# Kernel tuning notes

Hardware: AMD Instinct MI355X
Metric: run time of the kernel (lower is better)

The kernel has to match this reference:

```python
import jax, jax.numpy as jnp
import numpy as np

B, T, K, H = 8, 1024, 128, 8
TOP_K = 64
KS = 5  # conv kernel size for Q/K
DN = ('NCH', 'OIH', 'NCH')


def setup_inputs() -> dict:
    key = jax.random.key(0)
    ks = jax.random.split(key, 9)
    s = 0.05
    return {
        'x': jax.random.normal(ks[0], (B, T, K), jnp.float32),
        'Wq': jax.random.normal(ks[1], (K * H, K, KS), jnp.float32) * s,
        'bq': jax.random.normal(ks[2], (K * H,), jnp.float32) * s,
        'Wk': jax.random.normal(ks[3], (K * H, K, KS), jnp.float32) * s,
        'bk': jax.random.normal(ks[4], (K * H,), jnp.float32) * s,
        'Wv': jax.random.normal(ks[5], (K * H, K, 1), jnp.float32) * s,
        'bv': jax.random.normal(ks[6], (K * H,), jnp.float32) * s,
        'Wu': jax.random.normal(ks[7], (K, K * H), jnp.float32) * s,
        'bu': jax.random.normal(ks[8], (K,), jnp.float32) * s,
    }


def _prep(z, b, k, h, t, scale):
    # z: (b, k*h, t) conv output; torch view(b,k,h,t) then transposes -> (b,h,t,k)
    z = z.reshape(b, k, h, t)
    z = jnp.transpose(z, (0, 2, 3, 1)) * scale  # (b, h, t, k)
    # torch: transpose(1,2).contiguous().view(b*h, t, k) -- replicate exactly
    z = jnp.transpose(z, (0, 2, 1, 3)).reshape(b * h, t, k)
    return z


def reference(x, Wq, bq, Wk, bk, Wv, bv, Wu, bu):
    b, t, k = x.shape
    h = H
    xc = jnp.transpose(x, (0, 2, 1))  # (b, k, t)
    # causal left-pad KS-1 for Q/K convs; V is pointwise (kernel 1)
    q = jax.lax.conv_general_dilated(xc, Wq, (1,), [(KS - 1, 0)], dimension_numbers=DN) + bq[None, :, None]
    kk = jax.lax.conv_general_dilated(xc, Wk, (1,), [(KS - 1, 0)], dimension_numbers=DN) + bk[None, :, None]
    v = jax.lax.conv_general_dilated(xc, Wv, (1,), [(0, 0)], dimension_numbers=DN) + bv[None, :, None]
    scale = k ** -0.25
    q = _prep(q, b, k, h, t, scale)
    kk = _prep(kk, b, k, h, t, scale)
    v = _prep(v, b, k, h, t, 1.0)
    w = jnp.einsum('btk,bsk->bts', q, kk)  # (b*h, t, t)
    # top-k sparsification: keep entries >= k-th largest per row, else row min
    largest, _ = jax.lax.top_k(w, TOP_K)
    thresh = jnp.min(largest, axis=-1, keepdims=True)
    row_min = jnp.min(w, axis=-1, keepdims=True)
    w = jnp.where(w >= thresh, w, row_min)
    # causal mask (strict upper triangle -> -inf)
    causal = jnp.triu(jnp.ones((t, t), bool), 1)
    w = jnp.where(causal[None], -jnp.inf, w)
    w = jax.nn.softmax(w, axis=-1)
    out = jnp.einsum('bts,bsk->btk', w, v)  # (b*h, t, k)
    out = out.reshape(b, h, t, k)
    out = jnp.transpose(out, (0, 2, 1, 3)).reshape(b, t, k * h)
    return out @ Wu.T + bu
```

## Files before the change

### kernel.cpp

```cpp
#include <hip/hip_runtime.h>
#include <hip/hip_fp16.h>
#include <cstdint>

using f16 = _Float16;
typedef __attribute__((ext_vector_type(8))) _Float16 f16x8;
typedef __attribute__((ext_vector_type(4))) _Float16 f16x4;
typedef __attribute__((ext_vector_type(4))) float f32x4;

#define MFMA16(a, b, c) __builtin_amdgcn_mfma_f32_16x16x32_f16((a), (b), (c), 0, 0, 0)

__device__ __forceinline__ f16x8 ldfrag(const f16* p) { return *(const f16x8*)p; }

__device__ __forceinline__ void dma16(const f16* g, f16* l) {
  __builtin_amdgcn_global_load_lds(
      (const __attribute__((address_space(1))) void*)g,
      (__attribute__((address_space(3))) void*)l, 16, 0, 0);
}
__device__ __forceinline__ void wait_vm0() {
  asm volatile("s_waitcnt vmcnt(0)" ::: "memory");
}
__device__ __forceinline__ void wait_lgkm0() {
  asm volatile("s_waitcnt lgkmcnt(0)" ::: "memory");
}
__device__ __forceinline__ void wait_vm4() {
  asm volatile("s_waitcnt vmcnt(4)" ::: "memory");
}
__device__ __forceinline__ void wait_vm2() {
  asm volatile("s_waitcnt vmcnt(2)" ::: "memory");
}

static const int64_t NX = 1048576;
static const int64_t NW = 655360;
static const int64_t NV = 131072;

__global__ __launch_bounds__(256) void k0_prep(
    const float* __restrict__ x, const float* __restrict__ Wq,
    const float* __restrict__ Wk, const float* __restrict__ Wv,
    const float* __restrict__ Wu,
    f16* __restrict__ xh, f16* __restrict__ xl,
    f16* __restrict__ Wqh, f16* __restrict__ Wql,
    f16* __restrict__ Wkh, f16* __restrict__ Wkl,
    f16* __restrict__ Wvb, f16* __restrict__ Wub) {
  int64_t i = (int64_t)blockIdx.x * 256 + threadIdx.x;
  if (i < NX) {
    const float v = x[i];
    const f16 h = (f16)v;
    xh[i] = h; xl[i] = (f16)(v - (float)h);
  } else if (i < NX + NW) {
    int64_t d = i - NX;
    int j = (int)(d >> 17);
    int rem = (int)(d & 131071);
    int o = rem >> 7, c = rem & 127;
    const float v = Wq[(int64_t)(o * 128 + c) * 5 + j];
    const f16 h = (f16)v;
    Wqh[d] = h; Wql[d] = (f16)(v - (float)h);
  } else if (i < NX + 2 * NW) {
    int64_t d = i - NX - NW;
    int j = (int)(d >> 17);
    int rem = (int)(d & 131071);
    int o = rem >> 7, c = rem & 127;
    const float v = Wk[(int64_t)(o * 128 + c) * 5 + j];
    const f16 h = (f16)v;
    Wkh[d] = h; Wkl[d] = (f16)(v - (float)h);
  } else if (i < NX + 2 * NW + NV) {
    int64_t d = i - NX - 2 * NW;
    Wvb[d] = (f16)Wv[d];
  } else {
    int64_t d = i - NX - 2 * NW - NV;
    Wub[d] = (f16)Wu[d];
  }
}

#define STAGE_QK(DST, PASS, VALEXPR)                                    \
  {                                                                     \
    __syncthreads();                                                    \
    _Pragma("unroll")                                                   \
    for (int nt = 0; nt < 8; ++nt) {                                    \
      const int o = o0 + nt * 16 + lo;                                  \
      const int kcl = (o >> 3) & 63, hh = o & 7;                        \
      _Pragma("unroll")                                                 \
      for (int rtl = 0; rtl < 2; ++rtl) {                               \
        const int rt = (PASS) * 2 + rtl;                                \
        _Pragma("unroll")                                               \
        for (int r = 0; r < 4; ++r) {                                   \
          const int t2l = (rtl * 16 + quad * 4 + r) * 8 + hh;           \
          lds[t2l * 72 + kcl] = (VALEXPR);                              \
        }                                                               \
      }                                                                 \
    }                                                                   \
    __syncthreads();                                                    \
    _Pragma("unroll")                                                   \
    for (int p = 0; p < 8; ++p) {                                       \
      const int idx = p * 256 + tid;                                    \
      const int a = idx >> 3, c8 = (idx & 7) * 8;                       \
      *(f16x8*)(DST + ((int64_t)m * 1024 + t2b + (PASS) * 256 + a) * 128 + \
                half * 64 + c8) = *(const f16x8*)&lds[a * 72 + c8];     \
    }                                                                   \
  }

__global__ __launch_bounds__(256) void k1_conv(
    const f16* __restrict__ xh, const f16* __restrict__ xl,
    const f16* __restrict__ Wqh, const f16* __restrict__ Wql,
    const f16* __restrict__ Wkh, const f16* __restrict__ Wkl,
    const f16* __restrict__ Wvb,
    const float* __restrict__ bq, const float* __restrict__ bk,
    const float* __restrict__ bv,
    f16* __restrict__ q3h, f16* __restrict__ q3l,
    f16* __restrict__ k3h, f16* __restrict__ k3l,
    f16* __restrict__ v3T) {
  __shared__ f16 shm[36384];
  f16* const wbuf = shm;
  f16* const xbuf = shm + 18432;
  f16* const lds  = shm;
  const int tid = threadIdx.x;
  const int w = tid >> 6, lane = tid & 63;
  const int quad = lane >> 4, lo = lane & 15;
  const int r0 = blockIdx.x * 64;
  const int bb = r0 >> 10;
  const int m  = r0 >> 7;
  const int t2b = (r0 & 127) * 8;
  const int tloc = r0 & 1023;
  const int half = blockIdx.y;
  const int isK = blockIdx.z;
  const int o0 = half * 512 + w * 128;

  const f16* Wh = isK ? Wkh : Wqh;
  const f16* Wl = isK ? Wkl : Wql;
  const float* bias = isK ? bk : bq;

#pragma unroll
  for (int p = 0; p < 9; ++p) {
    const int u = p * 256 + tid;
    if (u < 2176) {
      const int row = u >> 5, tz = (u >> 4) & 1, c8 = (u & 15) * 8;
      int lt = tloc - 4 + row;
      if (lt < 0) lt = 0;
      const f16* src = (tz ? xl : xh) + ((int64_t)(bb * 1024 + lt)) * 128 + c8;
      *(f16x8*)&xbuf[row * 264 + tz * 128 + c8] = *(const f16x8*)src;
    }
  }
  __syncthreads();

  const int64_t wlane = (int64_t)(lane & 15) * 128 + (lane >> 4) * 8;

  if (!isK) {
    f32x4 av[4][8];
#pragma unroll
    for (int rt = 0; rt < 4; ++rt)
#pragma unroll
      for (int i = 0; i < 8; ++i)
#pragma unroll
        for (int r = 0; r < 4; ++r) av[rt][i][r] = 0.f;

#pragma unroll
    for (int g = 0; g < 4; ++g) {
#pragma unroll
      for (int s = 0; s < 2; ++s) {
        const int64_t vsrc = (int64_t)(o0 + (g * 2 + s) * 16) * 128 + wlane;
#pragma unroll
        for (int kk = 0; kk < 4; ++kk)
          dma16(Wvb + vsrc + kk * 32, wbuf + w * 4096 + s * 2048 + kk * 512);
      }
      wait_vm0();
#pragma unroll
      for (int kk = 0; kk < 4; ++kk) {
        f16x8 a[4];
#pragma unroll
        for (int rt = 0; rt < 4; ++rt)
          a[rt] = *(const f16x8*)&xbuf[(rt * 16 + lo + 4) * 264 + kk * 32 +
                                       quad * 8];
#pragma unroll
        for (int s = 0; s < 2; ++s) {
          const f16x8 bv8 = *(const f16x8*)&wbuf[w * 4096 + s * 2048 + kk * 512 +
                                                 quad * 128 + lo * 8];
#pragma unroll
          for (int rt = 0; rt < 4; ++rt)
            av[rt][g * 2 + s] = MFMA16(a[rt], bv8, av[rt][g * 2 + s]);
        }
      }
      wait_lgkm0();
    }
    __syncthreads();
#pragma unroll
    for (int pass = 0; pass < 2; ++pass) {
#pragma unroll
      for (int nt = 0; nt < 8; ++nt) {
        const int o = o0 + nt * 16 + lo;
        const float vbv = bv[o];
        const int kcl = (o >> 3) & 63, hh = o & 7;
#pragma unroll
        for (int rtl = 0; rtl < 2; ++rtl)
#pragma unroll
          for (int r = 0; r < 4; ++r) {
            const int t2l = (rtl * 16 + quad * 4 + r) * 8 + hh;
            lds[kcl * 264 + t2l] = (f16)(av[pass * 2 + rtl][nt][r] + vbv);
          }
      }
      __syncthreads();
#pragma unroll
      for (int p = 0; p < 8; ++p) {
        const int idx = p * 256 + tid;
        const int kcl = idx >> 5, t8 = (idx & 31) * 8;
        *(f16x8*)(v3T + ((int64_t)m * 128 + half * 64 + kcl) * 1024 + t2b +
                  pass * 256 + t8) = *(const f16x8*)&lds[kcl * 264 + t8];
      }
      __syncthreads();
    }
  }

  f32x4 aq[4][8];
#pragma unroll
  for (int rt = 0; rt < 4; ++rt)
#pragma unroll
    for (int i = 0; i < 8; ++i)
#pragma unroll
      for (int r = 0; r < 4; ++r) { aq[rt][i][r] = 0.f; }

  const int64_t wbase = wlane + (int64_t)o0 * 128;
#define ISSUE_HALF(J, KK, NTG, H)                                       \
  {                                                                     \
    _Pragma("unroll")                                                   \
    for (int ntl2 = 0; ntl2 < 2; ++ntl2) {                              \
      const int ntl_ = (H) * 2 + ntl2;                                  \
      const int64_t o_ = wbase + (int64_t)(J) * 131072 + (KK) * 32 +    \
                         (int64_t)(((NTG) * 4 + ntl_) * 16) * 128;      \
      dma16(Wh + o_, wbuf + w * 4096 + ntl_ * 1024);                    \
      dma16(Wl + o_, wbuf + w * 4096 + ntl_ * 1024 + 512);              \
    }                                                                   \
  }

  ISSUE_HALF(0, 0, 0, 0)
  ISSUE_HALF(0, 0, 0, 1)

  const bool z0 = (tloc == 0);
  for (int j = 0; j < 5; ++j) {
    f16x8 ah[4], al[4];
#pragma unroll
    for (int c = 0; c < 8; ++c) {
      const int kk = c >> 1, ntg = c & 1;
      if (ntg == 0) {
#pragma unroll
        for (int rt = 0; rt < 4; ++rt) {
          ah[rt] = *(const f16x8*)&xbuf[(rt * 16 + lo + j) * 264 + kk * 32 +
                                        quad * 8];
          al[rt] = *(const f16x8*)&xbuf[(rt * 16 + lo + j) * 264 + 128 +
                                        kk * 32 + quad * 8];
        }
        if (z0 && (lo + j < 4)) {
#pragma unroll
          for (int e = 0; e < 8; ++e) { ah[0][e] = (f16)0; al[0][e] = (f16)0; }
        }
      }
      const int nj = (c == 7) ? j + 1 : j;
      const int nkk = (c == 7) ? 0 : ((c + 1) >> 1);
      const int nntg = (c == 7) ? 0 : ((c + 1) & 1);
      const bool more = (c < 7) || (j < 4);

      wait_vm4();
#pragma unroll
      for (int ntl = 0; ntl < 2; ++ntl) {
        const int nt = ntg * 4 + ntl;
        const f16x8 bh = *(const f16x8*)&wbuf[w * 4096 + ntl * 1024 +
                                              quad * 128 + lo * 8];
        const f16x8 bl = *(const f16x8*)&wbuf[w * 4096 + ntl * 1024 + 512 +
                                              quad * 128 + lo * 8];
#pragma unroll
        for (int rt = 0; rt < 4; ++rt) {
          aq[rt][nt] = MFMA16(ah[rt], bh, aq[rt][nt]);
          aq[rt][nt] = MFMA16(ah[rt], bl, aq[rt][nt]);
          aq[rt][nt] = MFMA16(al[rt], bh, aq[rt][nt]);
        }
      }
      wait_lgkm0();
      if (more) ISSUE_HALF(nj, nkk, nntg, 0)

      if (c == 7) {
        if (j == 4) wait_vm0(); else wait_vm4();
      } else {
        wait_vm4();
      }
#pragma unroll
      for (int ntl = 2; ntl < 4; ++ntl) {
        const int nt = ntg * 4 + ntl;
        const f16x8 bh = *(const f16x8*)&wbuf[w * 4096 + ntl * 1024 +
                                              quad * 128 + lo * 8];
        const f16x8 bl = *(const f16x8*)&wbuf[w * 4096 + ntl * 1024 + 512 +
                                              quad * 128 + lo * 8];
#pragma unroll
        for (int rt = 0; rt < 4; ++rt) {
          aq[rt][nt] = MFMA16(ah[rt], bh, aq[rt][nt]);
          aq[rt][nt] = MFMA16(ah[rt], bl, aq[rt][nt]);
          aq[rt][nt] = MFMA16(al[rt], bh, aq[rt][nt]);
        }
      }
      wait_lgkm0();
      if (more) ISSUE_HALF(nj, nkk, nntg, 1)
    }
  }
#undef ISSUE_HALF

  const float SC = 0.29730177875068026f;
#pragma unroll
  for (int nt = 0; nt < 8; ++nt) {
    const int o = o0 + nt * 16 + lo;
    const float vb = bias[o];
#pragma unroll
    for (int rt = 0; rt < 4; ++rt)
#pragma unroll
      for (int r = 0; r < 4; ++r) aq[rt][nt][r] = (aq[rt][nt][r] + vb) * SC;
  }

  if (!isK) {
    STAGE_QK(q3h, 0, (f16)aq[rt][nt][r])
    STAGE_QK(q3h, 1, (f16)aq[rt][nt][r])
    STAGE_QK(q3l, 0, (f16)(aq[rt][nt][r] - (float)(f16)aq[rt][nt][r]))
    STAGE_QK(q3l, 1, (f16)(aq[rt][nt][r] - (float)(f16)aq[rt][nt][r]))
  } else {
    STAGE_QK(k3h, 0, (f16)aq[rt][nt][r])
    STAGE_QK(k3h, 1, (f16)aq[rt][nt][r])
    STAGE_QK(k3l, 0, (f16)(aq[rt][nt][r] - (float)(f16)aq[rt][nt][r]))
    STAGE_QK(k3l, 1, (f16)(aq[rt][nt][r] - (float)(f16)aq[rt][nt][r]))
  }
}

__global__ __launch_bounds__(512, 4) void k234_attn(
    const f16* __restrict__ q3h, const f16* __restrict__ q3l,
    const f16* __restrict__ k3h, const f16* __restrict__ k3l,
    const f16* __restrict__ v3T, f16* __restrict__ A) {
  __shared__ float Sb[16 * 516];
  __shared__ f16 kbuf[16384];
  const int tid = threadIdx.x;
  const int w = tid >> 6, lane = tid & 63;
  const int quad = lane >> 4, lo = lane & 15;
  const int qd = lane & 3, cit = lane >> 2;
  const int qsw = qd ^ ((cit >> 1) & 3);
  const int fro = (lo * 4 + (quad ^ ((lo >> 1) & 3))) * 8;
  const int hid = blockIdx.y * 64 + blockIdx.x;
  const int m = (hid & 7) * 8 + ((hid >> 3) >> 6);
  const int r0 = ((hid >> 3) & 63) * 16;

  const int64_t qoff = ((int64_t)m * 1024 + r0 + lo) * 128;
  f16x8 qh[4], ql[4];
#pragma unroll
  for (int kk = 0; kk < 4; ++kk) {
    qh[kk] = ldfrag(q3h + qoff + kk * 32 + quad * 8);
    ql[kk] = ldfrag(q3l + qoff + kk * 32 + quad * 8);
  }

  unsigned key[2][16];
  unsigned kmn0 = 0xFFFFFFFFu, kmn1 = 0xFFFFFFFFu;

#pragma unroll
  for (int half = 0; half < 2; ++half) {
    f32x4 acc[4];
#pragma unroll
    for (int i = 0; i < 4; ++i)
#pragma unroll
      for (int r = 0; r < 4; ++r) acc[i][r] = 0.f;

    for (int kp = 0; kp < 2; ++kp) {
#pragma unroll
      for (int cc = 0; cc < 4; ++cc) {
        const int c0 = half * 512 + cc * 128;
        const int64_t rowg = (int64_t)(m * 1024 + c0 + w * 16 + cit) * 128;
#pragma unroll
        for (int t = 0; t < 2; ++t) {
          const f16* srcb = t ? k3l : k3h;
#pragma unroll
          for (int kkh = 0; kkh < 2; ++kkh)
            dma16(srcb + rowg + (kp * 2 + kkh) * 32 + qsw * 8,
                  kbuf + (w * 4 + t * 2 + kkh) * 512);
        }
        wait_vm0();
#pragma unroll
        for (int kkh = 0; kkh < 2; ++kkh) {
          const int kkg = kp * 2 + kkh;
          f16x8 bh = *(const f16x8*)(kbuf + (w * 4 + kkh) * 512 + fro);
          f16x8 bl = *(const f16x8*)(kbuf + (w * 4 + 2 + kkh) * 512 + fro);
          acc[cc] = MFMA16(qh[kkg], bh, acc[cc]);
          acc[cc] = MFMA16(qh[kkg], bl, acc[cc]);
          acc[cc] = MFMA16(ql[kkg], bh, acc[cc]);
        }
        wait_lgkm0();
      }
    }
#pragma unroll
    for (int cc = 0; cc < 4; ++cc)
#pragma unroll
      for (int r = 0; r < 4; ++r)
        Sb[(quad * 4 + r) * 516 + cc * 128 + w * 16 + lo] = acc[cc][r];
    __syncthreads();
#pragma unroll
    for (int rr = 0; rr < 2; ++rr) {
      const float4* rp = (const float4*)(Sb + (w * 2 + rr) * 516);
#pragma unroll
      for (int i2 = 0; i2 < 2; ++i2) {
        const float4 f4 = rp[i2 * 64 + lane];
        const float fe[4] = {f4.x, f4.y, f4.z, f4.w};
#pragma unroll
        for (int e = 0; e < 4; ++e) {
          const unsigned u = __builtin_bit_cast(unsigned, fe[e]);
          const unsigned k = (u & 0x80000000u) ? ~u : (u | 0x80000000u);
          key[rr][half * 8 + i2 * 4 + e] = k;
          if (rr == 0) kmn0 = min(kmn0, k); else kmn1 = min(kmn1, k);
        }
      }
    }
    __syncthreads();
  }

  const int64_t vrow = (int64_t)(m * 128 + w * 16 + cit) * 1024;
  const int nkb = (r0 >> 6) + 1;
#define VISSUE(KB, PAIR)                                                 \
  {                                                                      \
    dma16(v3T + vrow + (KB) * 64 + qsw * 8,                              \
          kbuf + (w * 4 + (PAIR) * 2) * 512);                            \
    dma16(v3T + vrow + (KB) * 64 + 32 + qsw * 8,                         \
          kbuf + (w * 4 + (PAIR) * 2 + 1) * 512);                        \
  }
  VISSUE(0, 0)
  if (nkb > 1) VISSUE(1, 1)

  f16* P16 = (f16*)Sb;
  {
#pragma unroll
    for (int off = 32; off; off >>= 1) {
      kmn0 = min(kmn0, (unsigned)__shfl_xor((int)kmn0, off));
      kmn1 = min(kmn1, (unsigned)__shfl_xor((int)kmn1, off));
    }
    unsigned th0 = 0u, th1 = 0u;
    bool d0 = false, d1 = false;
    for (int b = 31; b >= 0; --b) {
      if (!d0) {
        const unsigned c0 = th0 | (1u << b);
        int cnt0 = 0;
#pragma unroll
        for (int i = 0; i < 16; ++i)
          cnt0 += (int)__popcll(__ballot(key[0][i] >= c0));
        if (cnt0 >= 64) { th0 = c0; if (cnt0 == 64) d0 = true; }
      }
      if (!d1) {
        const unsigned c1 = th1 | (1u << b);
        int cnt1 = 0;
#pragma unroll
        for (int i = 0; i < 16; ++i)
          cnt1 += (int)__popcll(__ballot(key[1][i] >= c1));
        if (cnt1 >= 64) { th1 = c1; if (cnt1 == 64) d1 = true; }
      }
      if (d0 && d1) break;
    }

#pragma unroll
    for (int rr = 0; rr < 2; ++rr) {
      const unsigned kth = rr ? th1 : th0;
      const unsigned kmn = rr ? kmn1 : kmn0;
      const int row = w * 2 + rr, t2 = r0 + row;
      const unsigned umn = (kmn & 0x80000000u) ? (kmn ^ 0x80000000u) : ~kmn;
      const float mn = __builtin_bit_cast(float, umn);
      const unsigned ukv = (kth & 0x80000000u) ? (kth ^ 0x80000000u) : ~kth;
      const float kv = __builtin_bit_cast(float, ukv);

      float ev[16];
      float sum = 0.f;
#pragma unroll
      for (int j = 0; j < 16; ++j) {
        const int s = (j >> 3) * 512 + ((j >> 2) & 1) * 256 + lane * 4 + (j & 3);
        const unsigned k = key[rr][j];
        const unsigned uu = (k & 0x80000000u) ? (k ^ 0x80000000u) : ~k;
        const float f = __builtin_bit_cast(float, uu);
        const float ww = (k >= kth) ? f : mn;
        const float x = (s <= t2) ? __expf(ww - kv) : 0.f;
        ev[j] = x;
        sum += x;
      }
      for (int off = 32; off; off >>= 1) sum += __shfl_xor(sum, off);
      const float inv = 1.0f / sum;

      f16* prow = P16 + row * 1032;
#pragma unroll
      for (int hh = 0; hh < 2; ++hh)
#pragma unroll
        for (int i2 = 0; i2 < 2; ++i2) {
          f16x4 pk;
#pragma unroll
          for (int e = 0; e < 4; ++e)
            pk[e] = (f16)(ev[hh * 8 + i2 * 4 + e] * inv);
          *(f16x4*)(prow + hh * 512 + i2 * 256 + lane * 4) = pk;
        }
    }
  }
  __syncthreads();

  {
    f32x4 oa0, oa1;
#pragma unroll
    for (int r = 0; r < 4; ++r) { oa0[r] = 0.f; oa1[r] = 0.f; }
    for (int kb = 0; kb < nkb; ++kb) {
      if (kb + 1 < nkb) wait_vm2();
      else wait_vm0();
      const int pair = kb & 1;
      {
        const f16x8 vf0 = *(const f16x8*)(kbuf + (w * 4 + pair * 2) * 512 + fro);
        const f16x8 vf1 =
            *(const f16x8*)(kbuf + (w * 4 + pair * 2 + 1) * 512 + fro);
        const f16x8 af0 = *(const f16x8*)(P16 + lo * 1032 + kb * 64 + quad * 8);
        const f16x8 af1 =
            *(const f16x8*)(P16 + lo * 1032 + kb * 64 + 32 + quad * 8);
        oa0 = MFMA16(af0, vf0, oa0);
        oa1 = MFMA16(af1, vf1, oa1);
      }
      wait_lgkm0();
      if (kb + 2 < nkb) VISSUE(kb + 2, pair)
    }
#undef VISSUE
#pragma unroll
    for (int r = 0; r < 4; ++r)
      A[((int64_t)m * 1024 + r0 + quad * 4 + r) * 128 + w * 16 + lo] =
          (f16)(oa0[r] + oa1[r]);
  }
}

__global__ __launch_bounds__(256) void k5_proj(
    const f16* __restrict__ A, const f16* __restrict__ Wub,
    const float* __restrict__ bu, float* __restrict__ out) {
  const int w = threadIdx.x >> 6, lane = threadIdx.x & 63;
  const int quad = lane >> 4, lo = lane & 15;
  const int rt = w & 1, ch = w >> 1;
  const int r0 = blockIdx.x * 32 + rt * 16;
  const int r = r0 + lo;
  const int bI = r >> 10, t2 = r & 1023;

  f32x4 acc[4];
#pragma unroll
  for (int i = 0; i < 4; ++i)
#pragma unroll
    for (int rr = 0; rr < 4; ++rr) acc[i][rr] = 0.f;

#pragma unroll 2
  for (int kk = 0; kk < 32; ++kk) {
    const int o = kk * 32 + quad * 8;
    const int j = o >> 7, kc = o & 127;
    f16x8 a = ldfrag(A + (((int64_t)(bI * 8 + j) * 1024 + t2) * 128 + kc));
    f16x8 wb[4];
#pragma unroll
    for (int nt = 0; nt < 4; ++nt)
      wb[nt] = ldfrag(Wub + (int64_t)(ch * 64 + nt * 16 + lo) * 1024 + o);
#pragma unroll
    for (int nt = 0; nt < 4; ++nt) acc[nt] = MFMA16(a, wb[nt], acc[nt]);
  }
#pragma unroll
  for (int nt = 0; nt < 4; ++nt) {
    const int col = ch * 64 + nt * 16 + lo;
    const float bias = bu[col];
#pragma unroll
    for (int rr = 0; rr < 4; ++rr) {
      const int row = r0 + quad * 4 + rr;
      out[(int64_t)row * 128 + col] = acc[nt][rr] + bias;
    }
  }
}

extern "C" void kernel_launch(void* const* d_in, const int* in_sizes, int n_in,
                              void* d_out, int out_size, void* d_ws, size_t ws_size,
                              hipStream_t stream) {
  const float* x  = (const float*)d_in[0];
  const float* Wq = (const float*)d_in[1];
  const float* bq = (const float*)d_in[2];
  const float* Wk = (const float*)d_in[3];
  const float* bk = (const float*)d_in[4];
  const float* Wv = (const float*)d_in[5];
  const float* bv = (const float*)d_in[6];
  const float* Wu = (const float*)d_in[7];
  const float* bu = (const float*)d_in[8];
  float* out = (float*)d_out;

  char* ws = (char*)d_ws;
  f16* xh  = (f16*)ws;  ws += 2097152;
  f16* xl  = (f16*)ws;  ws += 2097152;
  f16* Wqh = (f16*)ws;  ws += 1310720;
  f16* Wql = (f16*)ws;  ws += 1310720;
  f16* Wkh = (f16*)ws;  ws += 1310720;
  f16* Wkl = (f16*)ws;  ws += 1310720;
  f16* Wvb = (f16*)ws;  ws += 262144;
  f16* Wub = (f16*)ws;  ws += 262144;
  f16* q3h = (f16*)ws;  ws += 16777216;
  f16* q3l = (f16*)ws;  ws += 16777216;
  f16* k3h = (f16*)ws;  ws += 16777216;
  f16* k3l = (f16*)ws;  ws += 16777216;
  f16* v3T = (f16*)ws;  ws += 16777216;
  f16* A   = (f16*)ws;  ws += 16777216;

  k0_prep<<<10240, 256, 0, stream>>>(x, Wq, Wk, Wv, Wu,
                                     xh, xl, Wqh, Wql, Wkh, Wkl, Wvb, Wub);

  k1_conv<<<dim3(128, 2, 2), 256, 0, stream>>>(xh, xl, Wqh, Wql, Wkh, Wkl, Wvb,
                                               bq, bk, bv, q3h, q3l, k3h, k3l,
                                               v3T);

  k234_attn<<<dim3(64, 64), 512, 0, stream>>>(q3h, q3l, k3h, k3l, v3T, A);

  k5_proj<<<256, 256, 0, stream>>>(A, Wub, bu, out);

  (void)in_sizes; (void)n_in; (void)out_size; (void)ws_size;
}
```

Baseline: 408.2 us.

## Process two 16-row query groups per attention block to reuse K tiles

Each attention block now handles 32 query rows instead of 16, split into two groups, so every K tile staged into LDS feeds twice as many MFMAs. Q fragments are staged through a new LDS buffer per k-phase rather than held in registers. The top-k threshold search and the softmax/PV stages are run for both groups, and the grid is halved. This adds extra barriers, more LDS use, and more registers for the doubled keys and accumulators, which may lower occupancy. The Sb row padding is also removed, which may bring back LDS bank conflicts.

```diff
diff --git a/kernel.cpp b/kernel.cpp
--- a/kernel.cpp
+++ b/kernel.cpp
@@ -327,38 +327,48 @@
     const f16* __restrict__ q3h, const f16* __restrict__ q3l,
     const f16* __restrict__ k3h, const f16* __restrict__ k3l,
     const f16* __restrict__ v3T, f16* __restrict__ A) {
-  __shared__ float Sb[16 * 516];
+  __shared__ float Sb[16 * 512];
   __shared__ f16 kbuf[16384];
+  __shared__ f16 qlds[4096];
   const int tid = threadIdx.x;
   const int w = tid >> 6, lane = tid & 63;
   const int quad = lane >> 4, lo = lane & 15;
   const int qd = lane & 3, cit = lane >> 2;
   const int qsw = qd ^ ((cit >> 1) & 3);
   const int fro = (lo * 4 + (quad ^ ((lo >> 1) & 3))) * 8;
-  const int hid = blockIdx.y * 64 + blockIdx.x;
-  const int m = (hid & 7) * 8 + ((hid >> 3) >> 6);
-  const int r0 = ((hid >> 3) & 63) * 16;
-
-  const int64_t qoff = ((int64_t)m * 1024 + r0 + lo) * 128;
-  f16x8 qh[4], ql[4];
-#pragma unroll
-  for (int kk = 0; kk < 4; ++kk) {
-    qh[kk] = ldfrag(q3h + qoff + kk * 32 + quad * 8);
-    ql[kk] = ldfrag(q3l + qoff + kk * 32 + quad * 8);
-  }
-
-  unsigned key[2][16];
-  unsigned kmn0 = 0xFFFFFFFFu, kmn1 = 0xFFFFFFFFu;
+  const int hid = blockIdx.y * 32 + blockIdx.x;
+  const int m = (hid & 7) * 8 + ((hid >> 3) >> 5);
+  const int r0 = ((hid >> 3) & 31) * 32;
+
+  unsigned key[2][2][16];
+  unsigned kmn[2][2];
+#pragma unroll
+  for (int g = 0; g < 2; ++g)
+#pragma unroll
+    for (int rr = 0; rr < 2; ++rr) kmn[g][rr] = 0xFFFFFFFFu;
 
 #pragma unroll
   for (int half = 0; half < 2; ++half) {
-    f32x4 acc[4];
-#pragma unroll
-    for (int i = 0; i < 4; ++i)
-#pragma unroll
-      for (int r = 0; r < 4; ++r) acc[i][r] = 0.f;
+    f32x4 acc[2][4];
+#pragma unroll
+    for (int g = 0; g < 2; ++g)
+#pragma unroll
+      for (int i = 0; i < 4; ++i)
+#pragma unroll
+        for (int r = 0; r < 4; ++r) acc[g][i][r] = 0.f;
 
     for (int kp = 0; kp < 2; ++kp) {
+      __syncthreads();
+      {
+        const int h_ = w & 1, grp_ = (w >> 1) & 1, kkhs = (w >> 2) & 1;
+        const f16* qsrc = (h_ ? q3l : q3h) +
+            ((int64_t)m * 1024 + r0 + grp_ * 16 + lo) * 128 +
+            (kp * 2 + kkhs) * 32 + quad * 8;
+        dma16(qsrc, qlds + w * 512);
+        wait_vm0();
+      }
+      __syncthreads();
+
 #pragma unroll
       for (int cc = 0; cc < 4; ++cc) {
         const int c0 = half * 512 + cc * 128;
@@ -374,43 +384,53 @@
         wait_vm0();
 #pragma unroll
         for (int kkh = 0; kkh < 2; ++kkh) {
-          const int kkg = kp * 2 + kkh;
-          f16x8 bh = *(const f16x8*)(kbuf + (w * 4 + kkh) * 512 + fro);
-          f16x8 bl = *(const f16x8*)(kbuf + (w * 4 + 2 + kkh) * 512 + fro);
-          acc[cc] = MFMA16(qh[kkg], bh, acc[cc]);
-          acc[cc] = MFMA16(qh[kkg], bl, acc[cc]);
-          acc[cc] = MFMA16(ql[kkg], bh, acc[cc]);
+          const f16x8 qh0 = ldfrag(qlds + (kkh * 4 + 0) * 512 + lane * 8);
+          const f16x8 ql0 = ldfrag(qlds + (kkh * 4 + 1) * 512 + lane * 8);
+          const f16x8 qh1 = ldfrag(qlds + (kkh * 4 + 2) * 512 + lane * 8);
+          const f16x8 ql1 = ldfrag(qlds + (kkh * 4 + 3) * 512 + lane * 8);
+          const f16x8 bh = *(const f16x8*)(kbuf + (w * 4 + kkh) * 512 + fro);
+          const f16x8 bl =
+              *(const f16x8*)(kbuf + (w * 4 + 2 + kkh) * 512 + fro);
+          acc[0][cc] = MFMA16(qh0, bh, acc[0][cc]);
+          acc[0][cc] = MFMA16(qh0, bl, acc[0][cc]);
+          acc[0][cc] = MFMA16(ql0, bh, acc[0][cc]);
+          acc[1][cc] = MFMA16(qh1, bh, acc[1][cc]);
+          acc[1][cc] = MFMA16(qh1, bl, acc[1][cc]);
+          acc[1][cc] = MFMA16(ql1, bh, acc[1][cc]);
         }
         wait_lgkm0();
       }
     }
-#pragma unroll
-    for (int cc = 0; cc < 4; ++cc)
-#pragma unroll
-      for (int r = 0; r < 4; ++r)
-        Sb[(quad * 4 + r) * 516 + cc * 128 + w * 16 + lo] = acc[cc][r];
-    __syncthreads();
-#pragma unroll
-    for (int rr = 0; rr < 2; ++rr) {
-      const float4* rp = (const float4*)(Sb + (w * 2 + rr) * 516);
-#pragma unroll
-      for (int i2 = 0; i2 < 2; ++i2) {
-        const float4 f4 = rp[i2 * 64 + lane];
-        const float fe[4] = {f4.x, f4.y, f4.z, f4.w};
-#pragma unroll
-        for (int e = 0; e < 4; ++e) {
-          const unsigned u = __builtin_bit_cast(unsigned, fe[e]);
-          const unsigned k = (u & 0x80000000u) ? ~u : (u | 0x80000000u);
-          key[rr][half * 8 + i2 * 4 + e] = k;
-          if (rr == 0) kmn0 = min(kmn0, k); else kmn1 = min(kmn1, k);
-        }
-      }
-    }
-    __syncthreads();
+
+#pragma unroll
+    for (int grp = 0; grp < 2; ++grp) {
+#pragma unroll
+      for (int cc = 0; cc < 4; ++cc)
+#pragma unroll
+        for (int r = 0; r < 4; ++r)
+          Sb[(quad * 4 + r) * 512 + cc * 128 + w * 16 + lo] = acc[grp][cc][r];
+      __syncthreads();
+#pragma unroll
+      for (int rr = 0; rr < 2; ++rr) {
+        const float4* rp = (const float4*)(Sb + (w * 2 + rr) * 512);
+#pragma unroll
+        for (int i2 = 0; i2 < 2; ++i2) {
+          const float4 f4 = rp[i2 * 64 + lane];
+          const float fe[4] = {f4.x, f4.y, f4.z, f4.w};
+#pragma unroll
+          for (int e = 0; e < 4; ++e) {
+            const unsigned u = __builtin_bit_cast(unsigned, fe[e]);
+            const unsigned k = (u & 0x80000000u) ? ~u : (u | 0x80000000u);
+            key[grp][rr][half * 8 + i2 * 4 + e] = k;
+            kmn[grp][rr] = min(kmn[grp][rr], k);
+          }
+        }
+      }
+      __syncthreads();
+    }
   }
 
   const int64_t vrow = (int64_t)(m * 128 + w * 16 + cit) * 1024;
-  const int nkb = (r0 >> 6) + 1;
 #define VISSUE(KB, PAIR)                                                 \
   {                                                                      \
     dma16(v3T + vrow + (KB) * 64 + qsw * 8,                              \
@@ -419,43 +439,51 @@
           kbuf + (w * 4 + (PAIR) * 2 + 1) * 512);                        \
   }
   VISSUE(0, 0)
-  if (nkb > 1) VISSUE(1, 1)
+  if (r0 >= 64) VISSUE(1, 1)
+
+#pragma unroll
+  for (int off = 32; off; off >>= 1) {
+#pragma unroll
+    for (int g = 0; g < 2; ++g)
+#pragma unroll
+      for (int rr = 0; rr < 2; ++rr)
+        kmn[g][rr] = min(kmn[g][rr],
+                         (unsigned)__shfl_xor((int)kmn[g][rr], off));
+  }
+  unsigned th[2][2] = {{0u, 0u}, {0u, 0u}};
+  {
+    bool dn[2][2] = {{false, false}, {false, false}};
+    for (int b = 31; b >= 0; --b) {
+      bool all = true;
+#pragma unroll
+      for (int g = 0; g < 2; ++g)
+#pragma unroll
+        for (int rr = 0; rr < 2; ++rr) {
+          if (!dn[g][rr]) {
+            const unsigned c = th[g][rr] | (1u << b);
+            int cnt = 0;
+#pragma unroll
+            for (int i = 0; i < 16; ++i)
+              cnt += (int)__popcll(__ballot(key[g][rr][i] >= c));
+            if (cnt >= 64) { th[g][rr] = c; if (cnt == 64) dn[g][rr] = true; }
+          }
+          all = all && dn[g][rr];
+        }
+      if (all) break;
+    }
+  }
 
   f16* P16 = (f16*)Sb;
-  {
-#pragma unroll
-    for (int off = 32; off; off >>= 1) {
-      kmn0 = min(kmn0, (unsigned)__shfl_xor((int)kmn0, off));
-      kmn1 = min(kmn1, (unsigned)__shfl_xor((int)kmn1, off));
-    }
-    unsigned th0 = 0u, th1 = 0u;
-    bool d0 = false, d1 = false;
-    for (int b = 31; b >= 0; --b) {
-      if (!d0) {
-        const unsigned c0 = th0 | (1u << b);
-        int cnt0 = 0;
-#pragma unroll
-        for (int i = 0; i < 16; ++i)
-          cnt0 += (int)__popcll(__ballot(key[0][i] >= c0));
-        if (cnt0 >= 64) { th0 = c0; if (cnt0 == 64) d0 = true; }
-      }
-      if (!d1) {
-        const unsigned c1 = th1 | (1u << b);
-        int cnt1 = 0;
-#pragma unroll
-        for (int i = 0; i < 16; ++i)
-          cnt1 += (int)__popcll(__ballot(key[1][i] >= c1));
-        if (cnt1 >= 64) { th1 = c1; if (cnt1 == 64) d1 = true; }
-      }
-      if (d0 && d1) break;
-    }
-
+#pragma unroll
+  for (int grp = 0; grp < 2; ++grp) {
+    const int nkb = ((r0 + grp * 16) >> 6) + 1;
+    if (grp == 1) __syncthreads();
 #pragma unroll
     for (int rr = 0; rr < 2; ++rr) {
-      const unsigned kth = rr ? th1 : th0;
-      const unsigned kmn = rr ? kmn1 : kmn0;
-      const int row = w * 2 + rr, t2 = r0 + row;
-      const unsigned umn = (kmn & 0x80000000u) ? (kmn ^ 0x80000000u) : ~kmn;
+      const unsigned kth = th[grp][rr];
+      const unsigned kmv = kmn[grp][rr];
+      const int row = w * 2 + rr, t2 = r0 + grp * 16 + row;
+      const unsigned umn = (kmv & 0x80000000u) ? (kmv ^ 0x80000000u) : ~kmv;
       const float mn = __builtin_bit_cast(float, umn);
       const unsigned ukv = (kth & 0x80000000u) ? (kth ^ 0x80000000u) : ~kth;
       const float kv = __builtin_bit_cast(float, ukv);
@@ -465,7 +493,7 @@
 #pragma unroll
       for (int j = 0; j < 16; ++j) {
         const int s = (j >> 3) * 512 + ((j >> 2) & 1) * 256 + lane * 4 + (j & 3);
-        const unsigned k = key[rr][j];
+        const unsigned k = key[grp][rr][j];
         const unsigned uu = (k & 0x80000000u) ? (k ^ 0x80000000u) : ~k;
         const float f = __builtin_bit_cast(float, uu);
         const float ww = (k >= kth) ? f : mn;
@@ -476,7 +504,7 @@
       for (int off = 32; off; off >>= 1) sum += __shfl_xor(sum, off);
       const float inv = 1.0f / sum;
 
-      f16* prow = P16 + row * 1032;
+      f16* prow = P16 + row * 1024;
 #pragma unroll
       for (int hh = 0; hh < 2; ++hh)
 #pragma unroll
@@ -488,10 +516,8 @@
           *(f16x4*)(prow + hh * 512 + i2 * 256 + lane * 4) = pk;
         }
     }
-  }
-  __syncthreads();
-
-  {
+    __syncthreads();
+
     f32x4 oa0, oa1;
 #pragma unroll
     for (int r = 0; r < 4; ++r) { oa0[r] = 0.f; oa1[r] = 0.f; }
@@ -500,24 +526,29 @@
       else wait_vm0();
       const int pair = kb & 1;
       {
-        const f16x8 vf0 = *(const f16x8*)(kbuf + (w * 4 + pair * 2) * 512 + fro);
+        const f16x8 vf0 =
+            *(const f16x8*)(kbuf + (w * 4 + pair * 2) * 512 + fro);
         const f16x8 vf1 =
             *(const f16x8*)(kbuf + (w * 4 + pair * 2 + 1) * 512 + fro);
-        const f16x8 af0 = *(const f16x8*)(P16 + lo * 1032 + kb * 64 + quad * 8);
+        const f16x8 af0 = *(const f16x8*)(P16 + lo * 1024 + kb * 64 + quad * 8);
         const f16x8 af1 =
-            *(const f16x8*)(P16 + lo * 1032 + kb * 64 + 32 + quad * 8);
+            *(const f16x8*)(P16 + lo * 1024 + kb * 64 + 32 + quad * 8);
         oa0 = MFMA16(af0, vf0, oa0);
         oa1 = MFMA16(af1, vf1, oa1);
       }
       wait_lgkm0();
       if (kb + 2 < nkb) VISSUE(kb + 2, pair)
     }
+    if (grp == 0) {
+      VISSUE(0, 0)
+      if (((r0 + 16) >> 6) + 1 > 1) VISSUE(1, 1)
+    }
+#pragma unroll
+    for (int r = 0; r < 4; ++r)
+      A[((int64_t)m * 1024 + r0 + grp * 16 + quad * 4 + r) * 128 + w * 16 +
+        lo] = (f16)(oa0[r] + oa1[r]);
+  }
 #undef VISSUE
-#pragma unroll
-    for (int r = 0; r < 4; ++r)
-      A[((int64_t)m * 1024 + r0 + quad * 4 + r) * 128 + w * 16 + lo] =
-          (f16)(oa0[r] + oa1[r]);
-  }
 }
 
 __global__ __launch_bounds__(256) void k5_proj(
@@ -597,7 +628,7 @@
                                                bq, bk, bv, q3h, q3l, k3h, k3l,
                                                v3T);
 
-  k234_attn<<<dim3(64, 64), 512, 0, stream>>>(q3h, q3l, k3h, k3l, v3T, A);
+  k234_attn<<<dim3(32, 64), 512, 0, stream>>>(q3h, q3l, k3h, k3l, v3T, A);
 
   k5_proj<<<256, 256, 0, stream>>>(A, Wub, bu, out);
 
```

Result: no change. 411.7 us (+0.9%).
